# Optimization experiments

Hardware: AMD Instinct MI355X
Metric: run time of the kernel (lower is better)

The kernel has to match this reference:

```python
import jax, jax.numpy as jnp
import numpy as np

N_NODES = 100000
N_EDGES = 500000
E_DIM = 128  # embedding_channels
OUT_DIM = 1


def setup_inputs() -> dict:
    key = jax.random.key(0)
    k_z, k_ei, k_w1, k_w2 = jax.random.split(key, 4)
    z = jax.random.normal(k_z, (N_NODES, E_DIM), dtype=jnp.float32)
    edge_label_index = jax.random.randint(k_ei, (2, N_EDGES), 0, N_NODES, dtype=jnp.int64)
    # MLP([2E, E, out]) params, kaiming-ish scale
    W1 = jax.random.normal(k_w1, (2 * E_DIM, E_DIM), dtype=jnp.float32) * (2.0 / (2 * E_DIM)) ** 0.5
    b1 = jnp.zeros((E_DIM,), dtype=jnp.float32)
    W2 = jax.random.normal(k_w2, (E_DIM, OUT_DIM), dtype=jnp.float32) * (2.0 / E_DIM) ** 0.5
    b2 = jnpp = jnp.zeros((OUT_DIM,), dtype=jnp.float32)
    return {"z": z, "edge_label_index": edge_label_index,
            "W1": W1, "b1": b1, "W2": W2, "b2": b2}


def reference(z, edge_label_index, W1, b1, W2, b2):
    # gather endpoint embeddings and concat: [n_edges, 2E]
    src = z[edge_label_index[0]]  # [n_edges, E]
    dst = z[edge_label_index[1]]  # [n_edges, E]
    x = jnp.concatenate([src, dst], axis=-1)
    # MLP: Linear(2E->E) -> ReLU -> Linear(E->out)
    h = jax.nn.relu(x @ W1 + b1)
    return h @ W2 + b2
```

## Files before the change

### kernel.cpp

```cpp
#include <hip/hip_runtime.h>
#include <hip/hip_bf16.h>

#define N_NODES 100000
#define N_EDGES 500000

using bf16x8 = __attribute__((ext_vector_type(8))) __bf16;
using f32x4  = __attribute__((ext_vector_type(4))) float;


__global__ void cvt_w1f_kernel(const float* __restrict__ W1, __bf16* __restrict__ w1f) {
    int t = blockIdx.x * 256 + threadIdx.x;
    int lane = t & 63, frag = t >> 6;
    int kq = frag >> 4, c16 = frag & 15;
    int k0 = kq * 32 + (lane >> 4) * 8;
    int n  = c16 * 16 + (lane & 15);
    bf16x8 o;
#pragma unroll
    for (int i = 0; i < 8; i++) {
        int k = k0 + i;
        float w = (n < 128) ? W1[k * 128 + n] : W1[(k + 128) * 128 + (n - 128)];
        o[i] = (__bf16)w;
    }
    ((bf16x8*)w1f)[t] = o;
}

__global__ __launch_bounds__(256, 2) void node_gemm_kernel(
    const float* __restrict__ z, const __bf16* __restrict__ w1f,
    __bf16* __restrict__ C)
{
    __shared__ __bf16 sW[32 * 512];
    const int h = blockIdx.y;
    {
        const uint4* src = (const uint4*)w1f;
        uint4* dst = (uint4*)sW;
#pragma unroll
        for (int i = 0; i < 8; i++) {
            int u = threadIdx.x + 256 * i;
            int s = u >> 6, w = u & 63;
            int kq = s >> 3, nt = s & 7;
            dst[u] = src[(kq * 16 + h * 8 + nt) * 64 + w];
        }
    }
    __syncthreads();

    const int lane = threadIdx.x & 63;
    const int wave = threadIdx.x >> 6;
    const int l15 = lane & 15, l4 = lane >> 4;
    const int rowbase = blockIdx.x * 256 + wave * 64;

    const float* arow[4];
#pragma unroll
    for (int mt = 0; mt < 4; mt++) {
        int r = rowbase + mt * 16 + l15;
        if (r >= N_NODES) r = N_NODES - 1;
        arow[mt] = z + (size_t)r * 128 + l4 * 8;
    }

    const f32x4 zero = {0.f, 0.f, 0.f, 0.f};
    f32x4 acc[4][8];
#pragma unroll
    for (int mt = 0; mt < 4; mt++)
#pragma unroll
        for (int nt = 0; nt < 8; nt++) acc[mt][nt] = zero;

#pragma unroll
    for (int kq = 0; kq < 4; kq++) {
        bf16x8 bfr[8];
#pragma unroll
        for (int nt = 0; nt < 8; nt++)
            bfr[nt] = *(const bf16x8*)&sW[(kq * 8 + nt) * 512 + lane * 8];
#pragma unroll
        for (int mt = 0; mt < 4; mt++) {
            const float4* p = (const float4*)(arow[mt] + kq * 32);
            float4 x0 = p[0], x1 = p[1];
            bf16x8 a;
            a[0] = (__bf16)x0.x; a[1] = (__bf16)x0.y; a[2] = (__bf16)x0.z; a[3] = (__bf16)x0.w;
            a[4] = (__bf16)x1.x; a[5] = (__bf16)x1.y; a[6] = (__bf16)x1.z; a[7] = (__bf16)x1.w;
#pragma unroll
            for (int nt = 0; nt < 8; nt++)
                acc[mt][nt] = __builtin_amdgcn_mfma_f32_16x16x32_bf16(a, bfr[nt], acc[mt][nt], 0, 0, 0);
        }
    }

#pragma unroll
    for (int mt = 0; mt < 4; mt++) {
#pragma unroll
        for (int j = 0; j < 4; j++) {
            int r = rowbase + mt * 16 + l4 * 4 + j;
            if (r < N_NODES) {
                bf16x8 o;
#pragma unroll
                for (int nt = 0; nt < 8; nt++) o[nt] = (__bf16)acc[mt][nt][j];
                *(bf16x8*)(C + (size_t)r * 256 + h * 128 + l15 * 8) = o;
            }
        }
    }
}

__global__ __launch_bounds__(256, 6) void edge_kernel(
    const __bf16* __restrict__ C, const int* __restrict__ ei,
    const float* __restrict__ b1, const float* __restrict__ W2,
    const float* __restrict__ b2, float* __restrict__ out)
{
    const int lane = threadIdx.x & 63;
    const int wave = threadIdx.x >> 6;
    const int g = lane >> 4, sub = lane & 15;

    float b1v[8], w2v[8];
#pragma unroll
    for (int i = 0; i < 8; i++) {
        b1v[i] = b1[i * 16 + sub];
        w2v[i] = W2[i * 16 + sub];
    }
    const float bias2 = b2[0];

    const int wid = blockIdx.x * 4 + wave;
    const int nw  = gridDim.x * 4;

    for (int eb = wid * 16; eb < N_EDGES; eb += nw * 16) {
        bf16x8 cu[4], cv[4];
        int e[4];
#pragma unroll
        for (int q = 0; q < 4; q++) {
            e[q] = eb + q * 4 + g;
            int is = ei[e[q]];
            int id = ei[N_EDGES + e[q]];
            cu[q] = *(const bf16x8*)(C + (size_t)is * 256 + sub * 8);
            cv[q] = *(const bf16x8*)(C + (size_t)id * 256 + 128 + sub * 8);
        }
#pragma unroll
        for (int q = 0; q < 4; q++) {
            float p = 0.f;
#pragma unroll
            for (int i = 0; i < 8; i++) {
                float hc = (float)cu[q][i] + (float)cv[q][i] + b1v[i];
                p += fmaxf(hc, 0.f) * w2v[i];
            }
            p += __shfl_xor(p, 1, 64);
            p += __shfl_xor(p, 2, 64);
            p += __shfl_xor(p, 4, 64);
            p += __shfl_xor(p, 8, 64);
            if (sub == 0) out[e[q]] = p + bias2;
        }
    }
}

extern "C" void kernel_launch(void* const* d_in, const int* in_sizes, int n_in,
                              void* d_out, int out_size, void* d_ws, size_t ws_size,
                              hipStream_t stream) {
    const float* z  = (const float*)d_in[0];
    const int*   ei = (const int*)d_in[1];
    const float* W1 = (const float*)d_in[2];
    const float* b1 = (const float*)d_in[3];
    const float* W2 = (const float*)d_in[4];
    const float* b2 = (const float*)d_in[5];
    float* out = (float*)d_out;

    __bf16* w1f  = (__bf16*)d_ws;
    __bf16* Cbuf = (__bf16*)((char*)d_ws + 65536);

    cvt_w1f_kernel<<<16, 256, 0, stream>>>(W1, w1f);
    dim3 ggrid((N_NODES + 255) / 256, 2);
    node_gemm_kernel<<<ggrid, 256, 0, stream>>>(z, w1f, Cbuf);
    edge_kernel<<<2048, 256, 0, stream>>>(Cbuf, ei, b1, W2, b2, out);
}
```

Baseline: 149.7 us.

## Load node rows once for both weight halves and deepen edge gather batching

The node GEMM now loads and converts each z row fragment to bf16 once into registers and loops over both output halves inside one block. This halves z reads and drops the 2-wide grid. Weight fragments are read straight from global memory instead of being staged in LDS. The edge kernel batches 8 gather groups per wave iteration instead of 4 and uses half as many blocks, to keep more memory requests in flight. The cost is higher register pressure (afr plus acc arrays) and lower occupancy bounds.

```diff
diff --git a/kernel.cpp b/kernel.cpp
--- a/kernel.cpp
+++ b/kernel.cpp
@@ -28,76 +28,68 @@
     const float* __restrict__ z, const __bf16* __restrict__ w1f,
     __bf16* __restrict__ C)
 {
-    __shared__ __bf16 sW[32 * 512];
-    const int h = blockIdx.y;
-    {
-        const uint4* src = (const uint4*)w1f;
-        uint4* dst = (uint4*)sW;
-#pragma unroll
-        for (int i = 0; i < 8; i++) {
-            int u = threadIdx.x + 256 * i;
-            int s = u >> 6, w = u & 63;
-            int kq = s >> 3, nt = s & 7;
-            dst[u] = src[(kq * 16 + h * 8 + nt) * 64 + w];
-        }
-    }
-    __syncthreads();
-
     const int lane = threadIdx.x & 63;
     const int wave = threadIdx.x >> 6;
     const int l15 = lane & 15, l4 = lane >> 4;
     const int rowbase = blockIdx.x * 256 + wave * 64;
 
-    const float* arow[4];
+    bf16x8 afr[4][4];
 #pragma unroll
     for (int mt = 0; mt < 4; mt++) {
         int r = rowbase + mt * 16 + l15;
         if (r >= N_NODES) r = N_NODES - 1;
-        arow[mt] = z + (size_t)r * 128 + l4 * 8;
-    }
-
-    const f32x4 zero = {0.f, 0.f, 0.f, 0.f};
-    f32x4 acc[4][8];
+        const float* arow = z + (size_t)r * 128 + l4 * 8;
 #pragma unroll
-    for (int mt = 0; mt < 4; mt++)
-#pragma unroll
-        for (int nt = 0; nt < 8; nt++) acc[mt][nt] = zero;
-
-#pragma unroll
-    for (int kq = 0; kq < 4; kq++) {
-        bf16x8 bfr[8];
-#pragma unroll
-        for (int nt = 0; nt < 8; nt++)
-            bfr[nt] = *(const bf16x8*)&sW[(kq * 8 + nt) * 512 + lane * 8];
-#pragma unroll
-        for (int mt = 0; mt < 4; mt++) {
-            const float4* p = (const float4*)(arow[mt] + kq * 32);
+        for (int kq = 0; kq < 4; kq++) {
+            const float4* p = (const float4*)(arow + kq * 32);
             float4 x0 = p[0], x1 = p[1];
             bf16x8 a;
             a[0] = (__bf16)x0.x; a[1] = (__bf16)x0.y; a[2] = (__bf16)x0.z; a[3] = (__bf16)x0.w;
             a[4] = (__bf16)x1.x; a[5] = (__bf16)x1.y; a[6] = (__bf16)x1.z; a[7] = (__bf16)x1.w;
-#pragma unroll
-            for (int nt = 0; nt < 8; nt++)
-                acc[mt][nt] = __builtin_amdgcn_mfma_f32_16x16x32_bf16(a, bfr[nt], acc[mt][nt], 0, 0, 0);
+            afr[mt][kq] = a;
         }
     }
 
+    const f32x4 zero = {0.f, 0.f, 0.f, 0.f};
+
 #pragma unroll
-    for (int mt = 0; mt < 4; mt++) {
+    for (int h = 0; h < 2; h++) {
+        f32x4 acc[4][8];
 #pragma unroll
-        for (int j = 0; j < 4; j++) {
-            int r = rowbase + mt * 16 + l4 * 4 + j;
-            if (r < N_NODES) {
-                bf16x8 o;
+        for (int mt = 0; mt < 4; mt++)
 #pragma unroll
-                for (int nt = 0; nt < 8; nt++) o[nt] = (__bf16)acc[mt][nt][j];
-                *(bf16x8*)(C + (size_t)r * 256 + h * 128 + l15 * 8) = o;
+            for (int nt = 0; nt < 8; nt++) acc[mt][nt] = zero;
+
+#pragma unroll
+        for (int kq = 0; kq < 4; kq++) {
+            bf16x8 bfr[8];
+#pragma unroll
+            for (int nt = 0; nt < 8; nt++)
+                bfr[nt] = *(const bf16x8*)(w1f + ((kq * 16 + h * 8 + nt) * 64 + lane) * 8);
+#pragma unroll
+            for (int mt = 0; mt < 4; mt++)
+#pragma unroll
+                for (int nt = 0; nt < 8; nt++)
+                    acc[mt][nt] = __builtin_amdgcn_mfma_f32_16x16x32_bf16(afr[mt][kq], bfr[nt], acc[mt][nt], 0, 0, 0);
+        }
+
+#pragma unroll
+        for (int mt = 0; mt < 4; mt++) {
+#pragma unroll
+            for (int j = 0; j < 4; j++) {
+                int r = rowbase + mt * 16 + l4 * 4 + j;
+                if (r < N_NODES) {
+                    bf16x8 o;
+#pragma unroll
+                    for (int nt = 0; nt < 8; nt++) o[nt] = (__bf16)acc[mt][nt][j];
+                    *(bf16x8*)(C + (size_t)r * 256 + h * 128 + l15 * 8) = o;
+                }
             }
         }
     }
 }
 
-__global__ __launch_bounds__(256, 6) void edge_kernel(
+__global__ __launch_bounds__(256, 4) void edge_kernel(
     const __bf16* __restrict__ C, const int* __restrict__ ei,
     const float* __restrict__ b1, const float* __restrict__ W2,
     const float* __restrict__ b2, float* __restrict__ out)
@@ -117,11 +109,11 @@
     const int wid = blockIdx.x * 4 + wave;
     const int nw  = gridDim.x * 4;
 
-    for (int eb = wid * 16; eb < N_EDGES; eb += nw * 16) {
-        bf16x8 cu[4], cv[4];
-        int e[4];
+    for (int eb = wid * 32; eb < N_EDGES; eb += nw * 32) {
+        bf16x8 cu[8], cv[8];
+        int e[8];
 #pragma unroll
-        for (int q = 0; q < 4; q++) {
+        for (int q = 0; q < 8; q++) {
             e[q] = eb + q * 4 + g;
             int is = ei[e[q]];
             int id = ei[N_EDGES + e[q]];
@@ -129,7 +121,7 @@
             cv[q] = *(const bf16x8*)(C + (size_t)id * 256 + 128 + sub * 8);
         }
 #pragma unroll
-        for (int q = 0; q < 4; q++) {
+        for (int q = 0; q < 8; q++) {
             float p = 0.f;
 #pragma unroll
             for (int i = 0; i < 8; i++) {
@@ -160,7 +152,6 @@
     __bf16* Cbuf = (__bf16*)((char*)d_ws + 65536);
 
     cvt_w1f_kernel<<<16, 256, 0, stream>>>(W1, w1f);
-    dim3 ggrid((N_NODES + 255) / 256, 2);
-    node_gemm_kernel<<<ggrid, 256, 0, stream>>>(z, w1f, Cbuf);
-    edge_kernel<<<2048, 256, 0, stream>>>(Cbuf, ei, b1, W2, b2, out);
+    node_gemm_kernel<<<(N_NODES + 255) / 256, 256, 0, stream>>>(z, w1f, Cbuf);
+    edge_kernel<<<1024, 256, 0, stream>>>(Cbuf, ei, b1, W2, b2, out);
 }
```

Measured after the change: 160.9 us. +7.5%, slower.
